# Performance work log

Measured on AMD Instinct MI355X. Metric: run time of the kernel, lower is better.

## Reference

```python
import jax, jax.numpy as jnp
import numpy as np

NBITS = 4
GROUP_SIZE = 128


def setup_inputs() -> dict:
    key = jax.random.key(0)
    k1, k2, k3, k4, k5 = jax.random.split(key, 5)
    B, S, K, N = 2, 2048, 4096, 4096
    G = K // GROUP_SIZE  # 32 groups along K
    x = jax.random.normal(k1, (B, S, K), dtype=jnp.float16)
    # unpacked uint4 weights stored in int32 carrier, values in [0, 2^nbits)
    W_q = jax.random.randint(k2, (N, K), 0, 2 ** NBITS, dtype=jnp.int32)
    scale = (jax.random.uniform(k3, (N, G), dtype=jnp.float32) * 0.01 + 0.001).astype(jnp.float16)
    zero = (jax.random.uniform(k4, (N, G), dtype=jnp.float32) * (2 ** NBITS)).astype(jnp.float16)
    bias = jax.random.normal(k5, (N,), dtype=jnp.float16)
    return {"x": x, "W_q": W_q, "scale": scale, "zero": zero, "bias": bias}


def _dequant(W_q, scale, zero):
    # W_q: [N, K] int, scale/zero: [N, K//group_size] fp16
    # zeros_mode='original': W = (W_q - zero) * scale, per group along K
    N, K = W_q.shape
    G = K // GROUP_SIZE
    Wg = W_q.reshape(N, G, GROUP_SIZE).astype(jnp.float16)
    Wd = (Wg - zero[:, :, None]) * scale[:, :, None]
    return Wd.reshape(N, K)


def reference(x, W_q, scale, zero, bias):
    # out = x @ W_deq^T + bias   (layout 'nt': W is [N, K])
    W = _dequant(W_q, scale, zero)            # [N, K] fp16
    out = jnp.einsum('bsk,nk->bsn', x, W)     # [B, S, N] fp16 accum per module config
    return out + bias
```

## Files before the change

kernel.cpp:

```cpp
#include <hip/hip_runtime.h>
#include <hip/hip_bf16.h>


typedef __bf16 bf16x8 __attribute__((ext_vector_type(8)));
typedef float f32x4 __attribute__((ext_vector_type(4)));

#define BM 128
#define BN 128
#define BK 64

static __device__ __forceinline__ int pack_bf16x2(float a, float b) {
    __hip_bfloat162 p = __float22bfloat162_rn(make_float2(a, b));
    int r;
    __builtin_memcpy(&r, &p, 4);
    return r;
}

__global__ __launch_bounds__(256) void prepass_kernel(
    const float* __restrict__ X, unsigned short* __restrict__ Ad,
    const int*   __restrict__ Wq,
    const float* __restrict__ scale,
    const float* __restrict__ zero,
    unsigned short* __restrict__ Wd,
    int aUnits, int wUnits, int K, int G, int GROUP)
{
    const int stride = gridDim.x * blockDim.x;
    const int t0     = blockIdx.x * blockDim.x + threadIdx.x;

    for (int u = t0; u < aUnits; u += stride) {
        const long long f = (long long)u * 8;
        const float4 a0 = *(const float4*)(X + f);
        const float4 a1 = *(const float4*)(X + f + 4);
        int4 d;
        d.x = pack_bf16x2(a0.x, a0.y);
        d.y = pack_bf16x2(a0.z, a0.w);
        d.z = pack_bf16x2(a1.x, a1.y);
        d.w = pack_bf16x2(a1.z, a1.w);
        *(int4*)(Ad + f) = d;
    }

    const int unitsPerRow = K >> 3;
    for (int u = t0; u < wUnits; u += stride) {
        const int n = u / unitsPerRow;
        const int k = (u - n * unitsPerRow) * 8;
        const int g = k / GROUP;
        const float s  = scale[(long long)n * G + g];
        const float z  = zero [(long long)n * G + g];
        const float mz = -z * s;

        const long long f = (long long)n * K + k;
        const int4 q0 = *(const int4*)(Wq + f);
        const int4 q1 = *(const int4*)(Wq + f + 4);
        int4 d;
        d.x = pack_bf16x2((float)q0.x * s + mz, (float)q0.y * s + mz);
        d.y = pack_bf16x2((float)q0.z * s + mz, (float)q0.w * s + mz);
        d.z = pack_bf16x2((float)q1.x * s + mz, (float)q1.y * s + mz);
        d.w = pack_bf16x2((float)q1.z * s + mz, (float)q1.w * s + mz);
        *(int4*)(Wd + f) = d;
    }
}

#define KT 32
#define NRING 4

__global__ __launch_bounds__(512, 2) void gemm256_bf16_nt(
    const unsigned short* __restrict__ A,
    const unsigned short* __restrict__ Bw,
    const float* __restrict__ bias,
    float*       __restrict__ C,
    int M, int N, int K)
{
    __shared__ unsigned short ldsA[NRING][128 * 64];
    __shared__ unsigned short ldsB[NRING][128 * 64];

    const int tid  = threadIdx.x;
    const int lane = tid & 63;
    const int wave = tid >> 6;
    const int wm   = wave >> 2;
    const int wn   = wave & 3;

    const int nwg  = (N >> 8) * (M >> 8);
    const int cpx  = nwg >> 3;
    const int bid  = blockIdx.x;
    const int wgid = (bid & 7) * cpx + (bid >> 3);
    const int bx   = wgid % (N >> 8);
    const int by   = wgid / (N >> 8);
    const int blockN0 = bx << 8;
    const int blockM0 = by << 8;

    long long gOffA[2], gOffB[2];
    int ldsO[2];
#pragma unroll
    for (int l = 0; l < 2; ++l) {
        const int s  = l * 512 + tid;
        const int R  = s >> 3;
        const int j  = s & 7;
        const int ju = j ^ (R & 7);
        const int r  = 2 * R + (ju >> 2);
        const int c  = ju & 3;
        gOffA[l] = (long long)(blockM0 + r) * K + c * 8;
        gOffB[l] = (long long)(blockN0 + r) * K + c * 8;
        ldsO[l]  = (l * 512 + wave * 64) * 8;
    }

    const int row16 = lane & 15;
    const int quad  = lane >> 4;
    int offA[8], offB[4];
#pragma unroll
    for (int m = 0; m < 8; ++m) {
        const int r = wm * 128 + m * 16 + row16;
        const int R = r >> 1;
        const int j = ((r & 1) * 4 + quad) ^ (R & 7);
        offA[m] = R * 64 + j * 8;
    }
#pragma unroll
    for (int n = 0; n < 4; ++n) {
        const int r = wn * 64 + n * 16 + row16;
        const int R = r >> 1;
        const int j = ((r & 1) * 4 + quad) ^ (R & 7);
        offB[n] = R * 64 + j * 8;
    }

    f32x4 acc[8][4];
#pragma unroll
    for (int m = 0; m < 8; ++m)
#pragma unroll
        for (int n = 0; n < 4; ++n)
            acc[m][n] = (f32x4){0.f, 0.f, 0.f, 0.f};

#define STAGE(kt_, ring_)                                                     \
    do {                                                                      \
        const long long kOff_ = (long long)(kt_) * KT;                        \
        _Pragma("unroll")                                                     \
        for (int l = 0; l < 2; ++l) {                                         \
            __builtin_amdgcn_global_load_lds(                                 \
                (const __attribute__((address_space(1))) unsigned int*)       \
                    (A + gOffA[l] + kOff_),                                   \
                (__attribute__((address_space(3))) unsigned int*)             \
                    (&ldsA[ring_][ldsO[l]]),                                  \
                16, 0, 0);                                                    \
        }                                                                     \
        _Pragma("unroll")                                                     \
        for (int l = 0; l < 2; ++l) {                                         \
            __builtin_amdgcn_global_load_lds(                                 \
                (const __attribute__((address_space(1))) unsigned int*)       \
                    (Bw + gOffB[l] + kOff_),                                  \
                (__attribute__((address_space(3))) unsigned int*)             \
                    (&ldsB[ring_][ldsO[l]]),                                  \
                16, 0, 0);                                                    \
        }                                                                     \
    } while (0)

#define COMPUTE(ring_)                                                        \
    do {                                                                      \
        bf16x8 av[8], bv[4];                                                  \
        _Pragma("unroll")                                                     \
        for (int n = 0; n < 4; ++n)                                           \
            bv[n] = *(const bf16x8*)&ldsB[ring_][offB[n]];                    \
        _Pragma("unroll")                                                     \
        for (int m = 0; m < 8; ++m)                                           \
            av[m] = *(const bf16x8*)&ldsA[ring_][offA[m]];                    \
        __builtin_amdgcn_s_setprio(1);                                        \
        _Pragma("unroll")                                                     \
        for (int m = 0; m < 8; ++m)                                           \
            _Pragma("unroll")                                                 \
            for (int n = 0; n < 4; ++n)                                       \
                acc[m][n] = __builtin_amdgcn_mfma_f32_16x16x32_bf16(          \
                    av[m], bv[n], acc[m][n], 0, 0, 0);                        \
        __builtin_amdgcn_s_setprio(0);                                        \
    } while (0)

    const int NT = K / KT;

    STAGE(0, 0);
    STAGE(1, 1);
    STAGE(2, 2);

    for (int kt = 0; kt < NT - 3; ++kt) {
        __builtin_amdgcn_s_barrier();
        STAGE(kt + 3, (kt + 3) & 3);
        asm volatile("s_waitcnt vmcnt(8)" ::: "memory");
        __builtin_amdgcn_s_barrier();
        COMPUTE(kt & 3);
    }

    __builtin_amdgcn_s_barrier();
    asm volatile("s_waitcnt vmcnt(0)" ::: "memory");
    __builtin_amdgcn_s_barrier();
    COMPUTE((NT - 3) & 3);
    COMPUTE((NT - 2) & 3);
    COMPUTE((NT - 1) & 3);

#undef STAGE
#undef COMPUTE

    const int colBase = blockN0 + wn * 64;
    const int rowBase = blockM0 + wm * 128;
    float biasf[4];
#pragma unroll
    for (int n = 0; n < 4; ++n)
        biasf[n] = bias[colBase + n * 16 + row16];

#pragma unroll
    for (int m = 0; m < 8; ++m) {
        const int row0 = rowBase + m * 16 + quad * 4;
#pragma unroll
        for (int n = 0; n < 4; ++n) {
            const int col = colBase + n * 16 + row16;
#pragma unroll
            for (int r = 0; r < 4; ++r) {
                C[(long long)(row0 + r) * N + col] = acc[m][n][r] + biasf[n];
            }
        }
    }
}

__global__ __launch_bounds__(256, 2) void gemm_bf16_nt(
    const unsigned short* __restrict__ A,
    const unsigned short* __restrict__ Bw,
    const float* __restrict__ bias,
    float*       __restrict__ C,
    int M, int N, int K)
{
    __shared__ unsigned short ldsA[BM * BK];
    __shared__ unsigned short ldsB[BN * BK];

    const int tid   = threadIdx.x;
    const int lane  = tid & 63;
    const int wave  = tid >> 6;
    const int waveM = wave >> 1;
    const int waveN = wave & 1;

    const int blockN0 = blockIdx.x * BN;
    const int blockM0 = blockIdx.y * BM;

    const long long aBase = (long long)blockM0 * K;
    const long long bBase = (long long)blockN0 * K;

    const int rowInChunk = lane >> 3;
    const int colChunkSw = (lane & 7) ^ rowInChunk;
    const int col8       = colChunkSw * 8;

    f32x4 acc[4][4];
#pragma unroll
    for (int i = 0; i < 4; ++i)
#pragma unroll
        for (int j = 0; j < 4; ++j)
            acc[i][j] = (f32x4){0.f, 0.f, 0.f, 0.f};

    const int row16 = lane & 15;
    const int quad  = lane >> 4;
    const int sw    = row16 & 7;

    for (int k0 = 0; k0 < K; k0 += BK) {
        __syncthreads();
#pragma unroll
        for (int c = 0; c < 4; ++c) {
            const int chunk = (wave << 2) | c;
            const int row   = (chunk << 3) | rowInChunk;
            const unsigned short* gA = A  + aBase + (long long)row * K + k0 + col8;
            const unsigned short* gB = Bw + bBase + (long long)row * K + k0 + col8;
            __builtin_amdgcn_global_load_lds(
                (const __attribute__((address_space(1))) unsigned int*)gA,
                (__attribute__((address_space(3))) unsigned int*)&ldsA[chunk * 512],
                16, 0, 0);
            __builtin_amdgcn_global_load_lds(
                (const __attribute__((address_space(1))) unsigned int*)gB,
                (__attribute__((address_space(3))) unsigned int*)&ldsB[chunk * 512],
                16, 0, 0);
        }
        __syncthreads();

#pragma unroll
        for (int kk = 0; kk < 2; ++kk) {
            bf16x8 av[4], bv[4];
#pragma unroll
            for (int i = 0; i < 4; ++i) {
                const int r    = waveM * 64 + i * 16 + row16;
                const int slot = (kk * 4 + quad) ^ sw;
                av[i] = *(const bf16x8*)&ldsA[r * BK + slot * 8];
            }
#pragma unroll
            for (int j = 0; j < 4; ++j) {
                const int r    = waveN * 64 + j * 16 + row16;
                const int slot = (kk * 4 + quad) ^ sw;
                bv[j] = *(const bf16x8*)&ldsB[r * BK + slot * 8];
            }
#pragma unroll
            for (int i = 0; i < 4; ++i)
#pragma unroll
                for (int j = 0; j < 4; ++j)
                    acc[i][j] = __builtin_amdgcn_mfma_f32_16x16x32_bf16(
                        av[i], bv[j], acc[i][j], 0, 0, 0);
        }
    }

    const int colBase = blockN0 + waveN * 64;
    const int rowBase = blockM0 + waveM * 64;
    float biasf[4];
#pragma unroll
    for (int j = 0; j < 4; ++j)
        biasf[j] = bias[colBase + j * 16 + row16];

#pragma unroll
    for (int i = 0; i < 4; ++i) {
        const int row0 = rowBase + i * 16 + quad * 4;
#pragma unroll
        for (int j = 0; j < 4; ++j) {
            const int col = colBase + j * 16 + row16;
#pragma unroll
            for (int r = 0; r < 4; ++r) {
                C[(long long)(row0 + r) * N + col] = acc[i][j][r] + biasf[j];
            }
        }
    }
}

__global__ __launch_bounds__(256) void hqq_gemm_fused_f32(
    const float* __restrict__ A,
    const int*   __restrict__ Wq,
    const float* __restrict__ scale,
    const float* __restrict__ zero,
    const float* __restrict__ bias,
    float*       __restrict__ C,
    int M, int N, int K, int G, int GROUP)
{
    __shared__ unsigned short ldsA[BM * BK];
    __shared__ unsigned short ldsB[BN * BK];

    const int tid   = threadIdx.x;
    const int lane  = tid & 63;
    const int wave  = tid >> 6;
    const int waveM = wave >> 1;
    const int waveN = wave & 1;

    const int blockN0 = blockIdx.x * BN;
    const int blockM0 = blockIdx.y * BM;

    const int row16 = lane & 15;
    const int quad  = lane >> 4;

    f32x4 acc[4][4];
#pragma unroll
    for (int i = 0; i < 4; ++i)
#pragma unroll
        for (int j = 0; j < 4; ++j)
            acc[i][j] = (f32x4){0.f, 0.f, 0.f, 0.f};

    for (int k0 = 0; k0 < K; k0 += BK) {
        const int g = k0 / GROUP;
        int4 ra[4], rb[4];
#pragma unroll
        for (int c = 0; c < 4; ++c) {
            const int chunk = c * 256 + tid;
            const int row   = chunk >> 3;
            const int col   = (chunk & 7) * 8;

            const float* ap = A + (long long)(blockM0 + row) * K + k0 + col;
            const float4 a0 = *(const float4*)(ap);
            const float4 a1 = *(const float4*)(ap + 4);
            int4 da;
            da.x = pack_bf16x2(a0.x, a0.y);
            da.y = pack_bf16x2(a0.z, a0.w);
            da.z = pack_bf16x2(a1.x, a1.y);
            da.w = pack_bf16x2(a1.z, a1.w);
            ra[c] = da;

            const int n = blockN0 + row;
            const float s  = scale[(long long)n * G + g];
            const float z  = zero [(long long)n * G + g];
            const float mz = -z * s;
            const long long wb = (long long)n * K + k0 + col;
            const int4 q0 = *(const int4*)(Wq + wb);
            const int4 q1 = *(const int4*)(Wq + wb + 4);
            int4 db;
            db.x = pack_bf16x2((float)q0.x * s + mz, (float)q0.y * s + mz);
            db.y = pack_bf16x2((float)q0.z * s + mz, (float)q0.w * s + mz);
            db.z = pack_bf16x2((float)q1.x * s + mz, (float)q1.y * s + mz);
            db.w = pack_bf16x2((float)q1.z * s + mz, (float)q1.w * s + mz);
            rb[c] = db;
        }

        __syncthreads();
#pragma unroll
        for (int c = 0; c < 4; ++c) {
            const int chunk = c * 256 + tid;
            *(int4*)&ldsA[chunk * 8] = ra[c];
            *(int4*)&ldsB[chunk * 8] = rb[c];
        }
        __syncthreads();

#pragma unroll
        for (int kk = 0; kk < 2; ++kk) {
            const int kOff = kk * 32 + quad * 8;
            bf16x8 av[4], bv[4];
#pragma unroll
            for (int i = 0; i < 4; ++i)
                av[i] = *(const bf16x8*)&ldsA[(waveM * 64 + i * 16 + row16) * BK + kOff];
#pragma unroll
            for (int j = 0; j < 4; ++j)
                bv[j] = *(const bf16x8*)&ldsB[(waveN * 64 + j * 16 + row16) * BK + kOff];
#pragma unroll
            for (int i = 0; i < 4; ++i)
#pragma unroll
                for (int j = 0; j < 4; ++j)
                    acc[i][j] = __builtin_amdgcn_mfma_f32_16x16x32_bf16(
                        av[i], bv[j], acc[i][j], 0, 0, 0);
        }
    }

    const int colBase = blockN0 + waveN * 64;
    const int rowBase = blockM0 + waveM * 64;
    float biasf[4];
#pragma unroll
    for (int j = 0; j < 4; ++j)
        biasf[j] = bias[colBase + j * 16 + row16];

#pragma unroll
    for (int i = 0; i < 4; ++i) {
        const int row0 = rowBase + i * 16 + quad * 4;
#pragma unroll
        for (int j = 0; j < 4; ++j) {
            const int col = colBase + j * 16 + row16;
#pragma unroll
            for (int r = 0; r < 4; ++r) {
                C[(long long)(row0 + r) * N + col] = acc[i][j][r] + biasf[j];
            }
        }
    }
}

extern "C" void kernel_launch(void* const* d_in, const int* in_sizes, int n_in,
                              void* d_out, int out_size, void* d_ws, size_t ws_size,
                              hipStream_t stream) {
    (void)n_in; (void)out_size;

    const float* x     = (const float*)d_in[0];
    const int*   Wq    = (const int*)d_in[1];
    const float* scale = (const float*)d_in[2];
    const float* zero  = (const float*)d_in[3];
    const float* bias  = (const float*)d_in[4];
    float*       out   = (float*)d_out;

    const int N     = in_sizes[4];
    const int G     = in_sizes[2] / N;
    const int K     = in_sizes[1] / N;
    const int M     = in_sizes[0] / K;
    const int GROUP = K / G;

    const size_t needWs = (size_t)N * K * 2 + (size_t)M * K * 2;

    if (ws_size >= needWs) {
        unsigned short* Wd = (unsigned short*)d_ws;
        unsigned short* Ad = (unsigned short*)((char*)d_ws + (size_t)N * K * 2);

        const int aUnits = (int)((long long)M * K / 8);
        const int wUnits = (int)((long long)N * K / 8);
        prepass_kernel<<<2048, 256, 0, stream>>>(x, Ad, Wq, scale, zero, Wd,
                                                 aUnits, wUnits, K, G, GROUP);

        const int nwg = (N >> 8) * (M >> 8);
        if ((M % 256) == 0 && (N % 256) == 0 && (K % 128) == 0 && (nwg % 8) == 0) {
            gemm256_bf16_nt<<<nwg, 512, 0, stream>>>(Ad, Wd, bias, out, M, N, K);
        } else {
            dim3 grid(N / BN, M / BM);
            gemm_bf16_nt<<<grid, 256, 0, stream>>>(Ad, Wd, bias, out, M, N, K);
        }
    } else {
        dim3 grid(N / BN, M / BM);
        hqq_gemm_fused_f32<<<grid, 256, 0, stream>>>(x, Wq, scale, zero, bias, out,
                                                     M, N, K, G, GROUP);
    }
}
```

Before: 321.7 us.

## Restructure GEMM main loop into 8-phase interleaved load/compute pipeline

Replaces the 4-deep ring of 32-wide K stages with a double-buffered 64-wide K tile split into two halves. The main loop interleaves LDS fragment reads, partial global-to-LDS loads and half-tile MFMA groups across four barrier-separated phases. The aim is to overlap memory traffic and LDS reads with MFMA work at finer granularity than one big compute block per stage. LDS use per block stays the same, but there are more barriers per tile and the fragment registers are split into smaller groups, so the schedule is more fragile.

```diff
diff --git a/kernel.cpp b/kernel.cpp
--- a/kernel.cpp
+++ b/kernel.cpp
@@ -60,18 +60,15 @@
     }
 }
 
-#define KT 32
-#define NRING 4
-
-__global__ __launch_bounds__(512, 2) void gemm256_bf16_nt(
+__global__ __launch_bounds__(512, 2) void gemm256_8ph(
     const unsigned short* __restrict__ A,
     const unsigned short* __restrict__ Bw,
     const float* __restrict__ bias,
     float*       __restrict__ C,
     int M, int N, int K)
 {
-    __shared__ unsigned short ldsA[NRING][128 * 64];
-    __shared__ unsigned short ldsB[NRING][128 * 64];
+    __shared__ unsigned short ldsA[2][2][8192];
+    __shared__ unsigned short ldsB[2][2][8192];
 
     const int tid  = threadIdx.x;
     const int lane = tid & 63;
@@ -88,8 +85,8 @@
     const int blockN0 = bx << 8;
     const int blockM0 = by << 8;
 
-    long long gOffA[2], gOffB[2];
-    int ldsO[2];
+    long long gSrcA[2], gSrcB[2];
+    int ldsDst[2];
 #pragma unroll
     for (int l = 0; l < 2; ++l) {
         const int s  = l * 512 + tid;
@@ -97,10 +94,10 @@
         const int j  = s & 7;
         const int ju = j ^ (R & 7);
         const int r  = 2 * R + (ju >> 2);
-        const int c  = ju & 3;
-        gOffA[l] = (long long)(blockM0 + r) * K + c * 8;
-        gOffB[l] = (long long)(blockN0 + r) * K + c * 8;
-        ldsO[l]  = (l * 512 + wave * 64) * 8;
+        const int cc = ju & 3;
+        gSrcA[l] = (long long)(blockM0 + r) * K + cc * 8;
+        gSrcB[l] = (long long)(blockN0 + r) * K + cc * 8;
+        ldsDst[l] = (l * 512 + wave * 64) * 8;
     }
 
     const int row16 = lane & 15;
@@ -110,14 +107,14 @@
     for (int m = 0; m < 8; ++m) {
         const int r = wm * 128 + m * 16 + row16;
         const int R = r >> 1;
-        const int j = ((r & 1) * 4 + quad) ^ (R & 7);
+        const int j = (((r & 1) << 2) | quad) ^ (R & 7);
         offA[m] = R * 64 + j * 8;
     }
 #pragma unroll
     for (int n = 0; n < 4; ++n) {
         const int r = wn * 64 + n * 16 + row16;
         const int R = r >> 1;
-        const int j = ((r & 1) * 4 + quad) ^ (R & 7);
+        const int j = (((r & 1) << 2) | quad) ^ (R & 7);
         offB[n] = R * 64 + j * 8;
     }
 
@@ -128,71 +125,121 @@
         for (int n = 0; n < 4; ++n)
             acc[m][n] = (f32x4){0.f, 0.f, 0.f, 0.f};
 
-#define STAGE(kt_, ring_)                                                     \
+#define STAGE_A(T_, KH_)                                                      \
     do {                                                                      \
-        const long long kOff_ = (long long)(kt_) * KT;                        \
-        _Pragma("unroll")                                                     \
-        for (int l = 0; l < 2; ++l) {                                         \
-            __builtin_amdgcn_global_load_lds(                                 \
-                (const __attribute__((address_space(1))) unsigned int*)       \
-                    (A + gOffA[l] + kOff_),                                   \
-                (__attribute__((address_space(3))) unsigned int*)             \
-                    (&ldsA[ring_][ldsO[l]]),                                  \
-                16, 0, 0);                                                    \
-        }                                                                     \
-        _Pragma("unroll")                                                     \
-        for (int l = 0; l < 2; ++l) {                                         \
-            __builtin_amdgcn_global_load_lds(                                 \
-                (const __attribute__((address_space(1))) unsigned int*)       \
-                    (Bw + gOffB[l] + kOff_),                                  \
-                (__attribute__((address_space(3))) unsigned int*)             \
-                    (&ldsB[ring_][ldsO[l]]),                                  \
-                16, 0, 0);                                                    \
-        }                                                                     \
+        const int b_ = (T_) & 1;                                              \
+        const long long ko_ = (long long)(T_) * 64 + (KH_) * 32;              \
+        __builtin_amdgcn_global_load_lds(                                     \
+            (const __attribute__((address_space(1))) unsigned int*)           \
+                (A + gSrcA[0] + ko_),                                         \
+            (__attribute__((address_space(3))) unsigned int*)                 \
+                (&ldsA[b_][KH_][ldsDst[0]]), 16, 0, 0);                       \
+        __builtin_amdgcn_global_load_lds(                                     \
+            (const __attribute__((address_space(1))) unsigned int*)           \
+                (A + gSrcA[1] + ko_),                                         \
+            (__attribute__((address_space(3))) unsigned int*)                 \
+                (&ldsA[b_][KH_][ldsDst[1]]), 16, 0, 0);                       \
     } while (0)
 
-#define COMPUTE(ring_)                                                        \
+#define STAGE_B(T_, KH_)                                                      \
     do {                                                                      \
-        bf16x8 av[8], bv[4];                                                  \
-        _Pragma("unroll")                                                     \
-        for (int n = 0; n < 4; ++n)                                           \
-            bv[n] = *(const bf16x8*)&ldsB[ring_][offB[n]];                    \
-        _Pragma("unroll")                                                     \
-        for (int m = 0; m < 8; ++m)                                           \
-            av[m] = *(const bf16x8*)&ldsA[ring_][offA[m]];                    \
-        __builtin_amdgcn_s_setprio(1);                                        \
-        _Pragma("unroll")                                                     \
-        for (int m = 0; m < 8; ++m)                                           \
-            _Pragma("unroll")                                                 \
-            for (int n = 0; n < 4; ++n)                                       \
-                acc[m][n] = __builtin_amdgcn_mfma_f32_16x16x32_bf16(          \
-                    av[m], bv[n], acc[m][n], 0, 0, 0);                        \
-        __builtin_amdgcn_s_setprio(0);                                        \
+        const int b_ = (T_) & 1;                                              \
+        const long long ko_ = (long long)(T_) * 64 + (KH_) * 32;              \
+        __builtin_amdgcn_global_load_lds(                                     \
+            (const __attribute__((address_space(1))) unsigned int*)           \
+                (Bw + gSrcB[0] + ko_),                                        \
+            (__attribute__((address_space(3))) unsigned int*)                 \
+                (&ldsB[b_][KH_][ldsDst[0]]), 16, 0, 0);                       \
+        __builtin_amdgcn_global_load_lds(                                     \
+            (const __attribute__((address_space(1))) unsigned int*)           \
+                (Bw + gSrcB[1] + ko_),                                        \
+            (__attribute__((address_space(3))) unsigned int*)                 \
+                (&ldsB[b_][KH_][ldsDst[1]]), 16, 0, 0);                       \
     } while (0)
 
-    const int NT = K / KT;
-
-    STAGE(0, 0);
-    STAGE(1, 1);
-    STAGE(2, 2);
-
-    for (int kt = 0; kt < NT - 3; ++kt) {
+#define READ_BV(c_, kk_)                                                      \
+    bv0 = *(const bf16x8*)&ldsB[c_][kk_][offB[0]];                            \
+    bv1 = *(const bf16x8*)&ldsB[c_][kk_][offB[1]];                            \
+    bv2 = *(const bf16x8*)&ldsB[c_][kk_][offB[2]];                            \
+    bv3 = *(const bf16x8*)&ldsB[c_][kk_][offB[3]];
+
+#define READ_AV(c_, kk_, mh_)                                                 \
+    av0 = *(const bf16x8*)&ldsA[c_][kk_][offA[(mh_) * 4 + 0]];                \
+    av1 = *(const bf16x8*)&ldsA[c_][kk_][offA[(mh_) * 4 + 1]];                \
+    av2 = *(const bf16x8*)&ldsA[c_][kk_][offA[(mh_) * 4 + 2]];                \
+    av3 = *(const bf16x8*)&ldsA[c_][kk_][offA[(mh_) * 4 + 3]];
+
+#define MFROW(mi_, av_)                                                       \
+    acc[mi_][0] = __builtin_amdgcn_mfma_f32_16x16x32_bf16(av_, bv0, acc[mi_][0], 0, 0, 0); \
+    acc[mi_][1] = __builtin_amdgcn_mfma_f32_16x16x32_bf16(av_, bv1, acc[mi_][1], 0, 0, 0); \
+    acc[mi_][2] = __builtin_amdgcn_mfma_f32_16x16x32_bf16(av_, bv2, acc[mi_][2], 0, 0, 0); \
+    acc[mi_][3] = __builtin_amdgcn_mfma_f32_16x16x32_bf16(av_, bv3, acc[mi_][3], 0, 0, 0);
+
+#define MFMA16(mh_)                                                           \
+    __builtin_amdgcn_s_setprio(1);                                            \
+    MFROW((mh_) * 4 + 0, av0);                                                \
+    MFROW((mh_) * 4 + 1, av1);                                                \
+    MFROW((mh_) * 4 + 2, av2);                                                \
+    MFROW((mh_) * 4 + 3, av3);                                                \
+    __builtin_amdgcn_s_setprio(0);
+
+    const int NT = K >> 6;
+
+    STAGE_A(0, 0); STAGE_B(0, 0); STAGE_A(0, 1); STAGE_B(0, 1);
+    STAGE_A(1, 0); STAGE_B(1, 0); STAGE_A(1, 1);
+    asm volatile("s_waitcnt vmcnt(6)" ::: "memory");
+    __builtin_amdgcn_s_barrier();
+
+    bf16x8 av0, av1, av2, av3, bv0, bv1, bv2, bv3;
+
+#pragma unroll 2
+    for (int T = 0; T <= NT - 3; ++T) {
+        const int c = T & 1;
+        READ_BV(c, 0);
+        READ_AV(c, 0, 0);
+        STAGE_B(T + 1, 1);
         __builtin_amdgcn_s_barrier();
-        STAGE(kt + 3, (kt + 3) & 3);
-        asm volatile("s_waitcnt vmcnt(8)" ::: "memory");
+        MFMA16(0);
+        READ_AV(c, 0, 1);
+        STAGE_A(T + 2, 0);
         __builtin_amdgcn_s_barrier();
-        COMPUTE(kt & 3);
-    }
-
-    __builtin_amdgcn_s_barrier();
+        MFMA16(1);
+        READ_BV(c, 1);
+        READ_AV(c, 1, 0);
+        STAGE_B(T + 2, 0);
+        __builtin_amdgcn_s_barrier();
+        MFMA16(0);
+        READ_AV(c, 1, 1);
+        STAGE_A(T + 2, 1);
+        asm volatile("s_waitcnt vmcnt(6)" ::: "memory");
+        __builtin_amdgcn_s_barrier();
+        MFMA16(1);
+    }
+
+    STAGE_B(NT - 1, 1);
     asm volatile("s_waitcnt vmcnt(0)" ::: "memory");
     __builtin_amdgcn_s_barrier();
-    COMPUTE((NT - 3) & 3);
-    COMPUTE((NT - 2) & 3);
-    COMPUTE((NT - 1) & 3);
-
-#undef STAGE
-#undef COMPUTE
+    {
+        const int c = (NT - 2) & 1;
+        READ_BV(c, 0); READ_AV(c, 0, 0); MFMA16(0);
+        READ_AV(c, 0, 1); MFMA16(1);
+        READ_BV(c, 1); READ_AV(c, 1, 0); MFMA16(0);
+        READ_AV(c, 1, 1); MFMA16(1);
+    }
+    {
+        const int c = (NT - 1) & 1;
+        READ_BV(c, 0); READ_AV(c, 0, 0); MFMA16(0);
+        READ_AV(c, 0, 1); MFMA16(1);
+        READ_BV(c, 1); READ_AV(c, 1, 0); MFMA16(0);
+        READ_AV(c, 1, 1); MFMA16(1);
+    }
+
+#undef STAGE_A
+#undef STAGE_B
+#undef READ_BV
+#undef READ_AV
+#undef MFROW
+#undef MFMA16
 
     const int colBase = blockN0 + wn * 64;
     const int rowBase = blockM0 + wm * 128;
@@ -460,8 +507,10 @@
                                                  aUnits, wUnits, K, G, GROUP);
 
         const int nwg = (N >> 8) * (M >> 8);
-        if ((M % 256) == 0 && (N % 256) == 0 && (K % 128) == 0 && (nwg % 8) == 0) {
-            gemm256_bf16_nt<<<nwg, 512, 0, stream>>>(Ad, Wd, bias, out, M, N, K);
+        const int NT  = K >> 6;
+        if ((M % 256) == 0 && (N % 256) == 0 && (K % 64) == 0 && NT >= 4 &&
+            (nwg % 8) == 0) {
+            gemm256_8ph<<<nwg, 512, 0, stream>>>(Ad, Wd, bias, out, M, N, K);
         } else {
             dim3 grid(N / BN, M / BM);
             gemm_bf16_nt<<<grid, 256, 0, stream>>>(Ad, Wd, bias, out, M, N, K);
```

Result: faster. 283.9 us (-11.7%).
